# Optimization experiments

Measured on AMD Instinct MI355X. Metric: run time of the kernel, lower is better.

Reference implementation:

```python
import jax, jax.numpy as jnp
import numpy as np

N_NODES = 10000
N_EDGES = 640000
MODEL_DIM = 128
HIDDEN = [128, 128]


def setup_inputs() -> dict:
    key = jax.random.key(0)
    ks = jax.random.split(key, 10)
    node_feature = jax.random.normal(ks[0], (N_NODES, MODEL_DIM), dtype=jnp.float32)
    src = jax.random.randint(ks[1], (N_EDGES,), 0, N_NODES, dtype=jnp.int32)
    dst = jax.random.randint(ks[2], (N_EDGES,), 0, N_NODES, dtype=jnp.int32)
    in_dim = 2 * MODEL_DIM  # concat(aggregated_message, node_feature)
    # MLP: in_dim -> 128 -> 128 -> MODEL_DIM, ReLU between hidden layers
    W1 = jax.random.normal(ks[3], (in_dim, HIDDEN[0]), dtype=jnp.float32) / np.sqrt(in_dim)
    b1 = jnp.zeros((HIDDEN[0],), dtype=jnp.float32)
    W2 = jax.random.normal(ks[4], (HIDDEN[0], HIDDEN[1]), dtype=jnp.float32) / np.sqrt(HIDDEN[0])
    b2 = jnp.zeros((HIDDEN[1],), dtype=jnp.float32)
    W3 = jax.random.normal(ks[5], (HIDDEN[1], MODEL_DIM), dtype=jnp.float32) / np.sqrt(HIDDEN[1])
    b3 = jnp.zeros((MODEL_DIM,), dtype=jnp.float32)
    return {"node_feature": node_feature, "src": src, "dst": dst,
            "W1": W1, "b1": b1, "W2": W2, "b2": b2, "W3": W3, "b3": b3}


def reference(node_feature, src, dst, W1, b1, W2, b2, W3, b3):
    # message: gather src node features along edges  [E, D]
    # reduce: sum messages into dst nodes            [N, D]
    agg = jax.ops.segment_sum(node_feature[src], dst, num_segments=N_NODES)
    # apply_node_function_yes_neighbor: concat(aggregated_message, node_feature) -> MLP
    x = jnp.concatenate([agg, node_feature], axis=-1)  # [N, 2D]
    h = jax.nn.relu(x @ W1 + b1)
    h = jax.nn.relu(h @ W2 + b2)
    out = h @ W3 + b3  # [N, D]
    return out
```

## Files before the change

### kernel.cpp

```cpp
#include <hip/hip_runtime.h>
#include <hip/hip_bf16.h>

#define MODEL_D 128
#define CHUNK_SHIFT 13
#define CHUNK_SZ (1 << CHUNK_SHIFT)
#define CAPN 160
#define LDS_HIST 10240

typedef unsigned short ushort_t;
typedef unsigned int uint_t;
typedef __attribute__((ext_vector_type(8))) short short8v;
typedef __attribute__((ext_vector_type(4))) float f32x4;

static __device__ __forceinline__ ushort_t f2b(float v) {
    __hip_bfloat16 h = __float2bfloat16(v);
    return *reinterpret_cast<ushort_t*>(&h);
}

static __device__ __forceinline__ void acc8(float* acc, uint4 wv) {
    union { uint_t u32; float f; } lo, hi;
    lo.u32 = wv.x << 16;          acc[0] += lo.f;
    hi.u32 = wv.x & 0xffff0000u;  acc[1] += hi.f;
    lo.u32 = wv.y << 16;          acc[2] += lo.f;
    hi.u32 = wv.y & 0xffff0000u;  acc[3] += hi.f;
    lo.u32 = wv.z << 16;          acc[4] += lo.f;
    hi.u32 = wv.z & 0xffff0000u;  acc[5] += hi.f;
    lo.u32 = wv.w << 16;          acc[6] += lo.f;
    hi.u32 = wv.w & 0xffff0000u;  acc[7] += hi.f;
}

__global__ __launch_bounds__(1024) void histrank_convert_kernel(
    const int* __restrict__ dst, int* __restrict__ rank,
    int* __restrict__ hist2,
    const float* __restrict__ feat,
    const float* __restrict__ W1, const float* __restrict__ W2,
    const float* __restrict__ W3,
    ushort_t* __restrict__ featB, ushort_t* __restrict__ W1t,
    ushort_t* __restrict__ W2t, ushort_t* __restrict__ W3t,
    int E, int N, int nFeat, int C)
{
    __shared__ int h[LDS_HIST];
    const int t = threadIdx.x;
    const int c = blockIdx.x;

    if (c < C) {
        for (int i = t; i < N; i += 1024) h[i] = 0;
        __syncthreads();
        int e0 = c << CHUNK_SHIFT;
        int e1 = min(e0 + CHUNK_SZ, E);
        for (int e = e0 + t; e < e1; e += 1024)
            rank[e] = atomicAdd(&h[dst[e]], 1);
        __syncthreads();
        for (int i = t; i < N; i += 1024) hist2[(size_t)c * N + i] = h[i];
    }

    int gid = blockIdx.x * 1024 + t;
    int stride = gridDim.x * 1024;
    const int n1 = 256 * 128, n2 = 128 * 128, n3 = 128 * 128;
    int total = nFeat + n1 + n2 + n3;
    for (int i = gid; i < total; i += stride) {
        if (i < nFeat) {
            featB[i] = f2b(feat[i]);
        } else if (i < nFeat + n1) {
            int idx = i - nFeat; int j = idx >> 8, k = idx & 255;
            W1t[idx] = f2b(W1[k * 128 + j]);
        } else if (i < nFeat + n1 + n2) {
            int idx = i - nFeat - n1; int j = idx >> 7, k = idx & 127;
            W2t[idx] = f2b(W2[k * 128 + j]);
        } else {
            int idx = i - nFeat - n1 - n2; int j = idx >> 7, k = idx & 127;
            W3t[idx] = f2b(W3[k * 128 + j]);
        }
    }
}

__global__ __launch_bounds__(1024) void chunkscan_kernel(
    const int* __restrict__ hist2, int* __restrict__ chunkOff,
    int* __restrict__ deg, int N, int C)
{
    int node = blockIdx.x * 1024 + threadIdx.x;
    if (node >= N) return;
    int acc = 0;
    #pragma unroll 4
    for (int c = 0; c < C; ++c) {
        int v = hist2[(size_t)c * N + node];
        chunkOff[(size_t)c * N + node] = acc;
        acc += v;
    }
    deg[node] = acc;
}

__global__ __launch_bounds__(1024) void fill_kernel(
    const int* __restrict__ src, const int* __restrict__ dst,
    const int* __restrict__ rank, const int* __restrict__ chunkOff,
    int* __restrict__ srcSorted, int E, int N)
{
    int gid = blockIdx.x * 1024 + threadIdx.x;
    int stride = gridDim.x * 1024;
    for (int e = gid; e < E; e += stride) {
        int d = dst[e];
        int c = e >> CHUNK_SHIFT;
        int off = chunkOff[(size_t)c * N + d] + rank[e];
        if (off < CAPN) srcSorted[d * CAPN + off] = src[e];
    }
}

__global__ __launch_bounds__(512) void agg_mlp_kernel(
    const ushort_t* __restrict__ featB,
    const int* __restrict__ deg, const int* __restrict__ srcSorted,
    const ushort_t* __restrict__ W1t, const ushort_t* __restrict__ W2t,
    const ushort_t* __restrict__ W3t,
    const float* __restrict__ b1, const float* __restrict__ b2,
    const float* __restrict__ b3,
    float* __restrict__ out, int N)
{
    __shared__ ushort_t xsh[16][136];
    __shared__ ushort_t h1[16][136];
    __shared__ ushort_t h2[16][136];

    const int t = threadIdx.x;
    const int lane = t & 63;
    const int w = t >> 6;
    const int nb0 = blockIdx.x * 16;

    const int g4 = lane >> 4;
    const int c16 = lane & 15;
    const size_t cOff = c16 * 8;

    for (int q = 0; q < 2; ++q) {
        const int nl = w * 2 + q;
        const int node = nb0 + nl;
        float acc[8];
        #pragma unroll
        for (int j = 0; j < 8; ++j) acc[j] = 0.f;

        int degN = 0;
        if (node < N) {
            degN = deg[node];
            degN = (degN < CAPN) ? degN : CAPN;
        }
        const int sbase = node * CAPN;

        for (int chunk = 0; chunk < degN; chunk += 64) {
            int e = chunk + lane;
            int myidx = (e < degN) ? srcSorted[sbase + e] : 0;
            int nact = degN - chunk;
            nact = (nact < 64) ? nact : 64;
            int nfull = nact >> 2;

            int u = 0;
            for (; u + 4 <= nfull; u += 4) {
                int s0 = __shfl(myidx, (u + 0) * 4 + g4);
                int s1 = __shfl(myidx, (u + 1) * 4 + g4);
                int s2 = __shfl(myidx, (u + 2) * 4 + g4);
                int s3 = __shfl(myidx, (u + 3) * 4 + g4);
                uint4 wv0 = *(const uint4*)(featB + (size_t)s0 * MODEL_D + cOff);
                uint4 wv1 = *(const uint4*)(featB + (size_t)s1 * MODEL_D + cOff);
                uint4 wv2 = *(const uint4*)(featB + (size_t)s2 * MODEL_D + cOff);
                uint4 wv3 = *(const uint4*)(featB + (size_t)s3 * MODEL_D + cOff);
                acc8(acc, wv0);
                acc8(acc, wv1);
                acc8(acc, wv2);
                acc8(acc, wv3);
            }
            for (; u < nfull; ++u) {
                int s = __shfl(myidx, u * 4 + g4);
                uint4 wv = *(const uint4*)(featB + (size_t)s * MODEL_D + cOff);
                acc8(acc, wv);
            }
            int rem = nact & 3;
            if (rem) {
                bool valid = g4 < rem;
                int sel = valid ? (nfull * 4 + g4) : 0;
                int s = __shfl(myidx, sel);
                uint4 wv = *(const uint4*)(featB + (size_t)s * MODEL_D + cOff);
                if (valid) acc8(acc, wv);
            }
        }

        #pragma unroll
        for (int j = 0; j < 8; ++j) {
            acc[j] += __shfl_xor(acc[j], 16);
            acc[j] += __shfl_xor(acc[j], 32);
        }

        if (lane < 16) {
            uint4 o;
            o.x = (uint_t)f2b(acc[0]) | ((uint_t)f2b(acc[1]) << 16);
            o.y = (uint_t)f2b(acc[2]) | ((uint_t)f2b(acc[3]) << 16);
            o.z = (uint_t)f2b(acc[4]) | ((uint_t)f2b(acc[5]) << 16);
            o.w = (uint_t)f2b(acc[6]) | ((uint_t)f2b(acc[7]) << 16);
            *(uint4*)((char*)&xsh[nl][0] + c16 * 16) = o;
        }
    }
    __syncthreads();

    const int r16 = lane & 15;
    const int g = lane >> 4;
    const int ct = w;
    const int nodeA = nb0 + r16;
    const int nodeAc = (nodeA < N) ? nodeA : (N - 1);

    short8v a1f[8];
    {
        #pragma unroll
        for (int ks = 0; ks < 4; ++ks)
            a1f[ks] = *(const short8v*)&xsh[r16][ks * 32 + g * 8];
        #pragma unroll
        for (int ks = 0; ks < 4; ++ks)
            a1f[4 + ks] = *(const short8v*)(featB + (size_t)nodeAc * MODEL_D + ks * 32 + g * 8);

        f32x4 c = {0.f, 0.f, 0.f, 0.f};
        #pragma unroll
        for (int ks = 0; ks < 8; ++ks) {
            short8v b = *(const short8v*)(W1t + (ct * 16 + r16) * 256 + ks * 32 + g * 8);
            c = __builtin_amdgcn_mfma_f32_16x16x32_bf16(a1f[ks], b, c, 0, 0, 0);
        }
        const float bias = b1[ct * 16 + r16];
        #pragma unroll
        for (int i = 0; i < 4; ++i) {
            float v = fmaxf(c[i] + bias, 0.f);
            h1[g * 4 + i][ct * 16 + r16] = f2b(v);
        }
    }
    __syncthreads();

    {
        short8v a2f[4];
        #pragma unroll
        for (int ks = 0; ks < 4; ++ks)
            a2f[ks] = *(const short8v*)&h1[r16][ks * 32 + g * 8];
        f32x4 c = {0.f, 0.f, 0.f, 0.f};
        #pragma unroll
        for (int ks = 0; ks < 4; ++ks) {
            short8v b = *(const short8v*)(W2t + (ct * 16 + r16) * 128 + ks * 32 + g * 8);
            c = __builtin_amdgcn_mfma_f32_16x16x32_bf16(a2f[ks], b, c, 0, 0, 0);
        }
        const float bias = b2[ct * 16 + r16];
        #pragma unroll
        for (int i = 0; i < 4; ++i) {
            float v = fmaxf(c[i] + bias, 0.f);
            h2[g * 4 + i][ct * 16 + r16] = f2b(v);
        }
    }
    __syncthreads();

    {
        short8v a3f[4];
        #pragma unroll
        for (int ks = 0; ks < 4; ++ks)
            a3f[ks] = *(const short8v*)&h2[r16][ks * 32 + g * 8];
        f32x4 c = {0.f, 0.f, 0.f, 0.f};
        #pragma unroll
        for (int ks = 0; ks < 4; ++ks) {
            short8v b = *(const short8v*)(W3t + (ct * 16 + r16) * 128 + ks * 32 + g * 8);
            c = __builtin_amdgcn_mfma_f32_16x16x32_bf16(a3f[ks], b, c, 0, 0, 0);
        }
        const float bias = b3[ct * 16 + r16];
        #pragma unroll
        for (int i = 0; i < 4; ++i) {
            int node = nb0 + g * 4 + i;
            if (node < N)
                out[(size_t)node * MODEL_D + ct * 16 + r16] = c[i] + bias;
        }
    }
}

extern "C" void kernel_launch(void* const* d_in, const int* in_sizes, int n_in,
                              void* d_out, int out_size, void* d_ws, size_t ws_size,
                              hipStream_t stream) {
    const float* feat = (const float*)d_in[0];
    const int*   src  = (const int*)d_in[1];
    const int*   dst  = (const int*)d_in[2];
    const float* W1   = (const float*)d_in[3];
    const float* b1   = (const float*)d_in[4];
    const float* W2   = (const float*)d_in[5];
    const float* b2   = (const float*)d_in[6];
    const float* W3   = (const float*)d_in[7];
    const float* b3   = (const float*)d_in[8];
    float* out = (float*)d_out;

    const int N = in_sizes[0] / MODEL_D;
    const int E = in_sizes[1];
    const int NFEAT = N * MODEL_D;
    const int C = (E + CHUNK_SZ - 1) >> CHUNK_SHIFT;

    ushort_t* featB = (ushort_t*)d_ws;
    ushort_t* W1t   = featB + NFEAT;
    ushort_t* W2t   = W1t + 256 * 128;
    ushort_t* W3t   = W2t + 128 * 128;
    int* rank       = (int*)(W3t + 128 * 128);
    int* hist2      = rank + E;
    int* chunkOff   = hist2 + (size_t)C * N;
    int* deg        = chunkOff + (size_t)C * N;
    int* srcSorted  = deg + N;

    histrank_convert_kernel<<<625, 1024, 0, stream>>>(
        dst, rank, hist2, feat, W1, W2, W3,
        featB, W1t, W2t, W3t, E, N, NFEAT, C);

    chunkscan_kernel<<<(N + 1023) / 1024, 1024, 0, stream>>>(
        hist2, chunkOff, deg, N, C);

    fill_kernel<<<625, 1024, 0, stream>>>(
        src, dst, rank, chunkOff, srcSorted, E, N);

    agg_mlp_kernel<<<(N + 15) / 16, 512, 0, stream>>>(
        featB, deg, srcSorted, W1t, W2t, W3t, b1, b2, b3, out, N);
}
```

Measured before the change: 62.26 us.

## Split fused aggregation+MLP into separate gather kernel and 64-node MLP kernel

Splits the fused aggregate-and-MLP kernel into two kernels. The first gathers and sums neighbor features with one wave per node and writes the bf16 aggregate to workspace. The second runs the three-layer MLP on 64-node tiles, keeping weight fragments in registers and reusing them across four 16-row sub-tiles, which cuts repeated weight loads and removes the block-wide sync after the irregular gather. In exchange it adds an extra kernel launch and a round trip of the aggregate through global memory.

```diff
diff --git a/kernel.cpp b/kernel.cpp
--- a/kernel.cpp
+++ b/kernel.cpp
@@ -105,163 +105,202 @@
     }
 }
 
-__global__ __launch_bounds__(512) void agg_mlp_kernel(
+__global__ __launch_bounds__(256) void agg_kernel(
     const ushort_t* __restrict__ featB,
     const int* __restrict__ deg, const int* __restrict__ srcSorted,
+    ushort_t* __restrict__ aggB, int N)
+{
+    int gid = blockIdx.x * 256 + threadIdx.x;
+    int node = gid >> 6;
+    if (node >= N) return;
+    int lane = gid & 63;
+    const int g4 = lane >> 4;
+    const int c16 = lane & 15;
+    const size_t cOff = c16 * 8;
+
+    float acc[8];
+    #pragma unroll
+    for (int j = 0; j < 8; ++j) acc[j] = 0.f;
+
+    int degN = deg[node];
+    degN = (degN < CAPN) ? degN : CAPN;
+    const int sbase = node * CAPN;
+
+    for (int chunk = 0; chunk < degN; chunk += 64) {
+        int e = chunk + lane;
+        int myidx = (e < degN) ? srcSorted[sbase + e] : 0;
+        int nact = degN - chunk;
+        nact = (nact < 64) ? nact : 64;
+        int nfull = nact >> 2;
+
+        int u = 0;
+        for (; u + 4 <= nfull; u += 4) {
+            int s0 = __shfl(myidx, (u + 0) * 4 + g4);
+            int s1 = __shfl(myidx, (u + 1) * 4 + g4);
+            int s2 = __shfl(myidx, (u + 2) * 4 + g4);
+            int s3 = __shfl(myidx, (u + 3) * 4 + g4);
+            uint4 wv0 = *(const uint4*)(featB + (size_t)s0 * MODEL_D + cOff);
+            uint4 wv1 = *(const uint4*)(featB + (size_t)s1 * MODEL_D + cOff);
+            uint4 wv2 = *(const uint4*)(featB + (size_t)s2 * MODEL_D + cOff);
+            uint4 wv3 = *(const uint4*)(featB + (size_t)s3 * MODEL_D + cOff);
+            acc8(acc, wv0);
+            acc8(acc, wv1);
+            acc8(acc, wv2);
+            acc8(acc, wv3);
+        }
+        for (; u < nfull; ++u) {
+            int s = __shfl(myidx, u * 4 + g4);
+            uint4 wv = *(const uint4*)(featB + (size_t)s * MODEL_D + cOff);
+            acc8(acc, wv);
+        }
+        int rem = nact & 3;
+        if (rem) {
+            bool valid = g4 < rem;
+            int sel = valid ? (nfull * 4 + g4) : 0;
+            int s = __shfl(myidx, sel);
+            uint4 wv = *(const uint4*)(featB + (size_t)s * MODEL_D + cOff);
+            if (valid) acc8(acc, wv);
+        }
+    }
+
+    #pragma unroll
+    for (int j = 0; j < 8; ++j) {
+        acc[j] += __shfl_xor(acc[j], 16);
+        acc[j] += __shfl_xor(acc[j], 32);
+    }
+
+    if (lane < 16) {
+        uint4 o;
+        o.x = (uint_t)f2b(acc[0]) | ((uint_t)f2b(acc[1]) << 16);
+        o.y = (uint_t)f2b(acc[2]) | ((uint_t)f2b(acc[3]) << 16);
+        o.z = (uint_t)f2b(acc[4]) | ((uint_t)f2b(acc[5]) << 16);
+        o.w = (uint_t)f2b(acc[6]) | ((uint_t)f2b(acc[7]) << 16);
+        *(uint4*)(aggB + (size_t)node * MODEL_D + c16 * 8) = o;
+    }
+}
+
+__global__ __launch_bounds__(256) void mlp_kernel(
+    const ushort_t* __restrict__ aggB, const ushort_t* __restrict__ featB,
     const ushort_t* __restrict__ W1t, const ushort_t* __restrict__ W2t,
     const ushort_t* __restrict__ W3t,
     const float* __restrict__ b1, const float* __restrict__ b2,
     const float* __restrict__ b3,
     float* __restrict__ out, int N)
 {
-    __shared__ ushort_t xsh[16][136];
-    __shared__ ushort_t h1[16][136];
-    __shared__ ushort_t h2[16][136];
+    __shared__ ushort_t h1[64][136];
+    __shared__ ushort_t h2[64][136];
 
     const int t = threadIdx.x;
     const int lane = t & 63;
     const int w = t >> 6;
-    const int nb0 = blockIdx.x * 16;
-
-    const int g4 = lane >> 4;
-    const int c16 = lane & 15;
-    const size_t cOff = c16 * 8;
-
-    for (int q = 0; q < 2; ++q) {
-        const int nl = w * 2 + q;
-        const int node = nb0 + nl;
-        float acc[8];
-        #pragma unroll
-        for (int j = 0; j < 8; ++j) acc[j] = 0.f;
-
-        int degN = 0;
-        if (node < N) {
-            degN = deg[node];
-            degN = (degN < CAPN) ? degN : CAPN;
-        }
-        const int sbase = node * CAPN;
-
-        for (int chunk = 0; chunk < degN; chunk += 64) {
-            int e = chunk + lane;
-            int myidx = (e < degN) ? srcSorted[sbase + e] : 0;
-            int nact = degN - chunk;
-            nact = (nact < 64) ? nact : 64;
-            int nfull = nact >> 2;
-
-            int u = 0;
-            for (; u + 4 <= nfull; u += 4) {
-                int s0 = __shfl(myidx, (u + 0) * 4 + g4);
-                int s1 = __shfl(myidx, (u + 1) * 4 + g4);
-                int s2 = __shfl(myidx, (u + 2) * 4 + g4);
-                int s3 = __shfl(myidx, (u + 3) * 4 + g4);
-                uint4 wv0 = *(const uint4*)(featB + (size_t)s0 * MODEL_D + cOff);
-                uint4 wv1 = *(const uint4*)(featB + (size_t)s1 * MODEL_D + cOff);
-                uint4 wv2 = *(const uint4*)(featB + (size_t)s2 * MODEL_D + cOff);
-                uint4 wv3 = *(const uint4*)(featB + (size_t)s3 * MODEL_D + cOff);
-                acc8(acc, wv0);
-                acc8(acc, wv1);
-                acc8(acc, wv2);
-                acc8(acc, wv3);
-            }
-            for (; u < nfull; ++u) {
-                int s = __shfl(myidx, u * 4 + g4);
-                uint4 wv = *(const uint4*)(featB + (size_t)s * MODEL_D + cOff);
-                acc8(acc, wv);
-            }
-            int rem = nact & 3;
-            if (rem) {
-                bool valid = g4 < rem;
-                int sel = valid ? (nfull * 4 + g4) : 0;
-                int s = __shfl(myidx, sel);
-                uint4 wv = *(const uint4*)(featB + (size_t)s * MODEL_D + cOff);
-                if (valid) acc8(acc, wv);
-            }
-        }
-
-        #pragma unroll
-        for (int j = 0; j < 8; ++j) {
-            acc[j] += __shfl_xor(acc[j], 16);
-            acc[j] += __shfl_xor(acc[j], 32);
-        }
-
-        if (lane < 16) {
-            uint4 o;
-            o.x = (uint_t)f2b(acc[0]) | ((uint_t)f2b(acc[1]) << 16);
-            o.y = (uint_t)f2b(acc[2]) | ((uint_t)f2b(acc[3]) << 16);
-            o.z = (uint_t)f2b(acc[4]) | ((uint_t)f2b(acc[5]) << 16);
-            o.w = (uint_t)f2b(acc[6]) | ((uint_t)f2b(acc[7]) << 16);
-            *(uint4*)((char*)&xsh[nl][0] + c16 * 16) = o;
-        }
-    }
-    __syncthreads();
-
     const int r16 = lane & 15;
     const int g = lane >> 4;
-    const int ct = w;
-    const int nodeA = nb0 + r16;
-    const int nodeAc = (nodeA < N) ? nodeA : (N - 1);
-
-    short8v a1f[8];
+    const int nb0 = blockIdx.x * 64;
+
     {
-        #pragma unroll
-        for (int ks = 0; ks < 4; ++ks)
-            a1f[ks] = *(const short8v*)&xsh[r16][ks * 32 + g * 8];
-        #pragma unroll
-        for (int ks = 0; ks < 4; ++ks)
-            a1f[4 + ks] = *(const short8v*)(featB + (size_t)nodeAc * MODEL_D + ks * 32 + g * 8);
-
-        f32x4 c = {0.f, 0.f, 0.f, 0.f};
-        #pragma unroll
-        for (int ks = 0; ks < 8; ++ks) {
-            short8v b = *(const short8v*)(W1t + (ct * 16 + r16) * 256 + ks * 32 + g * 8);
-            c = __builtin_amdgcn_mfma_f32_16x16x32_bf16(a1f[ks], b, c, 0, 0, 0);
-        }
-        const float bias = b1[ct * 16 + r16];
-        #pragma unroll
-        for (int i = 0; i < 4; ++i) {
-            float v = fmaxf(c[i] + bias, 0.f);
-            h1[g * 4 + i][ct * 16 + r16] = f2b(v);
+        short8v B1[2][8];
+        float bias1[2];
+        #pragma unroll
+        for (int cc = 0; cc < 2; ++cc) {
+            const int ct = w * 2 + cc;
+            #pragma unroll
+            for (int ks = 0; ks < 8; ++ks)
+                B1[cc][ks] = *(const short8v*)(W1t + (ct * 16 + r16) * 256 + ks * 32 + g * 8);
+            bias1[cc] = b1[ct * 16 + r16];
+        }
+        #pragma unroll
+        for (int b = 0; b < 4; ++b) {
+            int nodeA = nb0 + b * 16 + r16;
+            int nodeAc = (nodeA < N) ? nodeA : (N - 1);
+            short8v a1f[8];
+            #pragma unroll
+            for (int ks = 0; ks < 4; ++ks)
+                a1f[ks] = *(const short8v*)(aggB + (size_t)nodeAc * MODEL_D + ks * 32 + g * 8);
+            #pragma unroll
+            for (int ks = 0; ks < 4; ++ks)
+                a1f[4 + ks] = *(const short8v*)(featB + (size_t)nodeAc * MODEL_D + ks * 32 + g * 8);
+            #pragma unroll
+            for (int cc = 0; cc < 2; ++cc) {
+                const int ct = w * 2 + cc;
+                f32x4 c = {0.f, 0.f, 0.f, 0.f};
+                #pragma unroll
+                for (int ks = 0; ks < 8; ++ks)
+                    c = __builtin_amdgcn_mfma_f32_16x16x32_bf16(a1f[ks], B1[cc][ks], c, 0, 0, 0);
+                #pragma unroll
+                for (int i = 0; i < 4; ++i) {
+                    float v = fmaxf(c[i] + bias1[cc], 0.f);
+                    h1[b * 16 + g * 4 + i][ct * 16 + r16] = f2b(v);
+                }
+            }
         }
     }
     __syncthreads();
 
     {
-        short8v a2f[4];
-        #pragma unroll
-        for (int ks = 0; ks < 4; ++ks)
-            a2f[ks] = *(const short8v*)&h1[r16][ks * 32 + g * 8];
-        f32x4 c = {0.f, 0.f, 0.f, 0.f};
-        #pragma unroll
-        for (int ks = 0; ks < 4; ++ks) {
-            short8v b = *(const short8v*)(W2t + (ct * 16 + r16) * 128 + ks * 32 + g * 8);
-            c = __builtin_amdgcn_mfma_f32_16x16x32_bf16(a2f[ks], b, c, 0, 0, 0);
-        }
-        const float bias = b2[ct * 16 + r16];
-        #pragma unroll
-        for (int i = 0; i < 4; ++i) {
-            float v = fmaxf(c[i] + bias, 0.f);
-            h2[g * 4 + i][ct * 16 + r16] = f2b(v);
+        short8v B2[2][4];
+        float bias2[2];
+        #pragma unroll
+        for (int cc = 0; cc < 2; ++cc) {
+            const int ct = w * 2 + cc;
+            #pragma unroll
+            for (int ks = 0; ks < 4; ++ks)
+                B2[cc][ks] = *(const short8v*)(W2t + (ct * 16 + r16) * 128 + ks * 32 + g * 8);
+            bias2[cc] = b2[ct * 16 + r16];
+        }
+        #pragma unroll
+        for (int b = 0; b < 4; ++b) {
+            short8v a2f[4];
+            #pragma unroll
+            for (int ks = 0; ks < 4; ++ks)
+                a2f[ks] = *(const short8v*)&h1[b * 16 + r16][ks * 32 + g * 8];
+            #pragma unroll
+            for (int cc = 0; cc < 2; ++cc) {
+                const int ct = w * 2 + cc;
+                f32x4 c = {0.f, 0.f, 0.f, 0.f};
+                #pragma unroll
+                for (int ks = 0; ks < 4; ++ks)
+                    c = __builtin_amdgcn_mfma_f32_16x16x32_bf16(a2f[ks], B2[cc][ks], c, 0, 0, 0);
+                #pragma unroll
+                for (int i = 0; i < 4; ++i) {
+                    float v = fmaxf(c[i] + bias2[cc], 0.f);
+                    h2[b * 16 + g * 4 + i][ct * 16 + r16] = f2b(v);
+                }
+            }
         }
     }
     __syncthreads();
 
     {
-        short8v a3f[4];
-        #pragma unroll
-        for (int ks = 0; ks < 4; ++ks)
-            a3f[ks] = *(const short8v*)&h2[r16][ks * 32 + g * 8];
-        f32x4 c = {0.f, 0.f, 0.f, 0.f};
-        #pragma unroll
-        for (int ks = 0; ks < 4; ++ks) {
-            short8v b = *(const short8v*)(W3t + (ct * 16 + r16) * 128 + ks * 32 + g * 8);
-            c = __builtin_amdgcn_mfma_f32_16x16x32_bf16(a3f[ks], b, c, 0, 0, 0);
-        }
-        const float bias = b3[ct * 16 + r16];
-        #pragma unroll
-        for (int i = 0; i < 4; ++i) {
-            int node = nb0 + g * 4 + i;
-            if (node < N)
-                out[(size_t)node * MODEL_D + ct * 16 + r16] = c[i] + bias;
+        short8v B3[2][4];
+        float bias3[2];
+        #pragma unroll
+        for (int cc = 0; cc < 2; ++cc) {
+            const int ct = w * 2 + cc;
+            #pragma unroll
+            for (int ks = 0; ks < 4; ++ks)
+                B3[cc][ks] = *(const short8v*)(W3t + (ct * 16 + r16) * 128 + ks * 32 + g * 8);
+            bias3[cc] = b3[ct * 16 + r16];
+        }
+        #pragma unroll
+        for (int b = 0; b < 4; ++b) {
+            short8v a3f[4];
+            #pragma unroll
+            for (int ks = 0; ks < 4; ++ks)
+                a3f[ks] = *(const short8v*)&h2[b * 16 + r16][ks * 32 + g * 8];
+            #pragma unroll
+            for (int cc = 0; cc < 2; ++cc) {
+                const int ct = w * 2 + cc;
+                f32x4 c = {0.f, 0.f, 0.f, 0.f};
+                #pragma unroll
+                for (int ks = 0; ks < 4; ++ks)
+                    c = __builtin_amdgcn_mfma_f32_16x16x32_bf16(a3f[ks], B3[cc][ks], c, 0, 0, 0);
+                #pragma unroll
+                for (int i = 0; i < 4; ++i) {
+                    int node = nb0 + b * 16 + g * 4 + i;
+                    if (node < N)
+                        out[(size_t)node * MODEL_D + ct * 16 + r16] = c[i] + bias3[cc];
+                }
+            }
         }
     }
 }
@@ -286,7 +325,8 @@
     const int C = (E + CHUNK_SZ - 1) >> CHUNK_SHIFT;
 
     ushort_t* featB = (ushort_t*)d_ws;
-    ushort_t* W1t   = featB + NFEAT;
+    ushort_t* aggB  = featB + NFEAT;
+    ushort_t* W1t   = aggB + NFEAT;
     ushort_t* W2t   = W1t + 256 * 128;
     ushort_t* W3t   = W2t + 128 * 128;
     int* rank       = (int*)(W3t + 128 * 128);
@@ -305,6 +345,9 @@
     fill_kernel<<<625, 1024, 0, stream>>>(
         src, dst, rank, chunkOff, srcSorted, E, N);
 
-    agg_mlp_kernel<<<(N + 15) / 16, 512, 0, stream>>>(
-        featB, deg, srcSorted, W1t, W2t, W3t, b1, b2, b3, out, N);
-}
+    agg_kernel<<<(N * 64 + 255) / 256, 256, 0, stream>>>(
+        featB, deg, srcSorted, aggB, N);
+
+    mlp_kernel<<<(N + 63) / 64, 256, 0, stream>>>(
+        aggB, featB, W1t, W2t, W3t, b1, b2, b3, out, N);
+}
```

Measured after the change: 59.94 us, median of 2. 1.04x faster.

## Split aggregation from MLP into separate kernels and unroll fill by four

Applied to the files above, without the earlier changes.

The fused aggregate+MLP kernel becomes two kernels. A standalone agg_kernel runs one wavefront per node in small blocks and writes bf16 aggregates to a new workspace buffer, and mlp_kernel reads them back from global memory. This targets poor latency hiding and load imbalance in the fused kernel, where each 512-thread block gathered 16 nodes before its MFMA stage. It costs an extra launch and a round trip of the aggregate through memory. Separately, fill_kernel now processes four strided edges per thread to raise memory-level parallelism.

```diff
diff --git a/kernel.cpp b/kernel.cpp
--- a/kernel.cpp
+++ b/kernel.cpp
@@ -96,8 +96,27 @@
     int* __restrict__ srcSorted, int E, int N)
 {
     int gid = blockIdx.x * 1024 + threadIdx.x;
+    int q = E >> 2;
     int stride = gridDim.x * 1024;
-    for (int e = gid; e < E; e += stride) {
+    for (int i = gid; i < q; i += stride) {
+        int e0 = i, e1 = i + q, e2 = i + 2 * q, e3 = i + 3 * q;
+        int d0 = dst[e0], d1 = dst[e1], d2 = dst[e2], d3 = dst[e3];
+        int r0 = rank[e0], r1 = rank[e1], r2 = rank[e2], r3 = rank[e3];
+        int c0 = e0 >> CHUNK_SHIFT, c1 = e1 >> CHUNK_SHIFT;
+        int c2 = e2 >> CHUNK_SHIFT, c3 = e3 >> CHUNK_SHIFT;
+        int o0 = chunkOff[(size_t)c0 * N + d0] + r0;
+        int o1 = chunkOff[(size_t)c1 * N + d1] + r1;
+        int o2 = chunkOff[(size_t)c2 * N + d2] + r2;
+        int o3 = chunkOff[(size_t)c3 * N + d3] + r3;
+        int s0 = src[e0], s1 = src[e1], s2 = src[e2], s3 = src[e3];
+        if (o0 < CAPN) srcSorted[d0 * CAPN + o0] = s0;
+        if (o1 < CAPN) srcSorted[d1 * CAPN + o1] = s1;
+        if (o2 < CAPN) srcSorted[d2 * CAPN + o2] = s2;
+        if (o3 < CAPN) srcSorted[d3 * CAPN + o3] = s3;
+    }
+    int rem = E - 4 * q;
+    if (gid < rem) {
+        int e = 4 * q + gid;
         int d = dst[e];
         int c = e >> CHUNK_SHIFT;
         int off = chunkOff[(size_t)c * N + d] + rank[e];
@@ -105,111 +124,109 @@
     }
 }
 
-__global__ __launch_bounds__(512) void agg_mlp_kernel(
+__global__ __launch_bounds__(256) void agg_kernel(
     const ushort_t* __restrict__ featB,
     const int* __restrict__ deg, const int* __restrict__ srcSorted,
+    ushort_t* __restrict__ aggB, int N)
+{
+    int gid = blockIdx.x * 256 + threadIdx.x;
+    int node = gid >> 6;
+    if (node >= N) return;
+    int lane = gid & 63;
+    const int g4 = lane >> 4;
+    const int c16 = lane & 15;
+    const size_t cOff = c16 * 8;
+
+    float acc[8];
+    #pragma unroll
+    for (int j = 0; j < 8; ++j) acc[j] = 0.f;
+
+    int degN = deg[node];
+    degN = (degN < CAPN) ? degN : CAPN;
+    const int sbase = node * CAPN;
+
+    for (int chunk = 0; chunk < degN; chunk += 64) {
+        int e = chunk + lane;
+        int myidx = (e < degN) ? srcSorted[sbase + e] : 0;
+        int nact = degN - chunk;
+        nact = (nact < 64) ? nact : 64;
+        int nfull = nact >> 2;
+
+        int u = 0;
+        for (; u + 4 <= nfull; u += 4) {
+            int s0 = __shfl(myidx, (u + 0) * 4 + g4);
+            int s1 = __shfl(myidx, (u + 1) * 4 + g4);
+            int s2 = __shfl(myidx, (u + 2) * 4 + g4);
+            int s3 = __shfl(myidx, (u + 3) * 4 + g4);
+            uint4 wv0 = *(const uint4*)(featB + (size_t)s0 * MODEL_D + cOff);
+            uint4 wv1 = *(const uint4*)(featB + (size_t)s1 * MODEL_D + cOff);
+            uint4 wv2 = *(const uint4*)(featB + (size_t)s2 * MODEL_D + cOff);
+            uint4 wv3 = *(const uint4*)(featB + (size_t)s3 * MODEL_D + cOff);
+            acc8(acc, wv0);
+            acc8(acc, wv1);
+            acc8(acc, wv2);
+            acc8(acc, wv3);
+        }
+        for (; u < nfull; ++u) {
+            int s = __shfl(myidx, u * 4 + g4);
+            uint4 wv = *(const uint4*)(featB + (size_t)s * MODEL_D + cOff);
+            acc8(acc, wv);
+        }
+        int rem = nact & 3;
+        if (rem) {
+            bool valid = g4 < rem;
+            int sel = valid ? (nfull * 4 + g4) : 0;
+            int s = __shfl(myidx, sel);
+            uint4 wv = *(const uint4*)(featB + (size_t)s * MODEL_D + cOff);
+            if (valid) acc8(acc, wv);
+        }
+    }
+
+    #pragma unroll
+    for (int j = 0; j < 8; ++j) {
+        acc[j] += __shfl_xor(acc[j], 16);
+        acc[j] += __shfl_xor(acc[j], 32);
+    }
+
+    if (lane < 16) {
+        uint4 o;
+        o.x = (uint_t)f2b(acc[0]) | ((uint_t)f2b(acc[1]) << 16);
+        o.y = (uint_t)f2b(acc[2]) | ((uint_t)f2b(acc[3]) << 16);
+        o.z = (uint_t)f2b(acc[4]) | ((uint_t)f2b(acc[5]) << 16);
+        o.w = (uint_t)f2b(acc[6]) | ((uint_t)f2b(acc[7]) << 16);
+        *(uint4*)(aggB + (size_t)node * MODEL_D + c16 * 8) = o;
+    }
+}
+
+__global__ __launch_bounds__(512) void mlp_kernel(
+    const ushort_t* __restrict__ aggB, const ushort_t* __restrict__ featB,
     const ushort_t* __restrict__ W1t, const ushort_t* __restrict__ W2t,
     const ushort_t* __restrict__ W3t,
     const float* __restrict__ b1, const float* __restrict__ b2,
     const float* __restrict__ b3,
     float* __restrict__ out, int N)
 {
-    __shared__ ushort_t xsh[16][136];
     __shared__ ushort_t h1[16][136];
     __shared__ ushort_t h2[16][136];
 
     const int t = threadIdx.x;
     const int lane = t & 63;
     const int w = t >> 6;
-    const int nb0 = blockIdx.x * 16;
-
-    const int g4 = lane >> 4;
-    const int c16 = lane & 15;
-    const size_t cOff = c16 * 8;
-
-    for (int q = 0; q < 2; ++q) {
-        const int nl = w * 2 + q;
-        const int node = nb0 + nl;
-        float acc[8];
-        #pragma unroll
-        for (int j = 0; j < 8; ++j) acc[j] = 0.f;
-
-        int degN = 0;
-        if (node < N) {
-            degN = deg[node];
-            degN = (degN < CAPN) ? degN : CAPN;
-        }
-        const int sbase = node * CAPN;
-
-        for (int chunk = 0; chunk < degN; chunk += 64) {
-            int e = chunk + lane;
-            int myidx = (e < degN) ? srcSorted[sbase + e] : 0;
-            int nact = degN - chunk;
-            nact = (nact < 64) ? nact : 64;
-            int nfull = nact >> 2;
-
-            int u = 0;
-            for (; u + 4 <= nfull; u += 4) {
-                int s0 = __shfl(myidx, (u + 0) * 4 + g4);
-                int s1 = __shfl(myidx, (u + 1) * 4 + g4);
-                int s2 = __shfl(myidx, (u + 2) * 4 + g4);
-                int s3 = __shfl(myidx, (u + 3) * 4 + g4);
-                uint4 wv0 = *(const uint4*)(featB + (size_t)s0 * MODEL_D + cOff);
-                uint4 wv1 = *(const uint4*)(featB + (size_t)s1 * MODEL_D + cOff);
-                uint4 wv2 = *(const uint4*)(featB + (size_t)s2 * MODEL_D + cOff);
-                uint4 wv3 = *(const uint4*)(featB + (size_t)s3 * MODEL_D + cOff);
-                acc8(acc, wv0);
-                acc8(acc, wv1);
-                acc8(acc, wv2);
-                acc8(acc, wv3);
-            }
-            for (; u < nfull; ++u) {
-                int s = __shfl(myidx, u * 4 + g4);
-                uint4 wv = *(const uint4*)(featB + (size_t)s * MODEL_D + cOff);
-                acc8(acc, wv);
-            }
-            int rem = nact & 3;
-            if (rem) {
-                bool valid = g4 < rem;
-                int sel = valid ? (nfull * 4 + g4) : 0;
-                int s = __shfl(myidx, sel);
-                uint4 wv = *(const uint4*)(featB + (size_t)s * MODEL_D + cOff);
-                if (valid) acc8(acc, wv);
-            }
-        }
-
-        #pragma unroll
-        for (int j = 0; j < 8; ++j) {
-            acc[j] += __shfl_xor(acc[j], 16);
-            acc[j] += __shfl_xor(acc[j], 32);
-        }
-
-        if (lane < 16) {
-            uint4 o;
-            o.x = (uint_t)f2b(acc[0]) | ((uint_t)f2b(acc[1]) << 16);
-            o.y = (uint_t)f2b(acc[2]) | ((uint_t)f2b(acc[3]) << 16);
-            o.z = (uint_t)f2b(acc[4]) | ((uint_t)f2b(acc[5]) << 16);
-            o.w = (uint_t)f2b(acc[6]) | ((uint_t)f2b(acc[7]) << 16);
-            *(uint4*)((char*)&xsh[nl][0] + c16 * 16) = o;
-        }
-    }
-    __syncthreads();
-
     const int r16 = lane & 15;
     const int g = lane >> 4;
     const int ct = w;
+    const int nb0 = blockIdx.x * 16;
     const int nodeA = nb0 + r16;
     const int nodeAc = (nodeA < N) ? nodeA : (N - 1);
 
-    short8v a1f[8];
     {
+        short8v a1f[8];
         #pragma unroll
         for (int ks = 0; ks < 4; ++ks)
-            a1f[ks] = *(const short8v*)&xsh[r16][ks * 32 + g * 8];
+            a1f[ks] = *(const short8v*)(aggB + (size_t)nodeAc * MODEL_D + ks * 32 + g * 8);
         #pragma unroll
         for (int ks = 0; ks < 4; ++ks)
             a1f[4 + ks] = *(const short8v*)(featB + (size_t)nodeAc * MODEL_D + ks * 32 + g * 8);
-
         f32x4 c = {0.f, 0.f, 0.f, 0.f};
         #pragma unroll
         for (int ks = 0; ks < 8; ++ks) {
@@ -286,7 +303,8 @@
     const int C = (E + CHUNK_SZ - 1) >> CHUNK_SHIFT;
 
     ushort_t* featB = (ushort_t*)d_ws;
-    ushort_t* W1t   = featB + NFEAT;
+    ushort_t* aggB  = featB + NFEAT;
+    ushort_t* W1t   = aggB + NFEAT;
     ushort_t* W2t   = W1t + 256 * 128;
     ushort_t* W3t   = W2t + 128 * 128;
     int* rank       = (int*)(W3t + 128 * 128);
@@ -302,9 +320,12 @@
     chunkscan_kernel<<<(N + 1023) / 1024, 1024, 0, stream>>>(
         hist2, chunkOff, deg, N, C);
 
-    fill_kernel<<<625, 1024, 0, stream>>>(
+    fill_kernel<<<((E >> 2) + 1023) / 1024, 1024, 0, stream>>>(
         src, dst, rank, chunkOff, srcSorted, E, N);
 
-    agg_mlp_kernel<<<(N + 15) / 16, 512, 0, stream>>>(
-        featB, deg, srcSorted, W1t, W2t, W3t, b1, b2, b3, out, N);
-}
+    agg_kernel<<<(N * 64 + 255) / 256, 256, 0, stream>>>(
+        featB, deg, srcSorted, aggB, N);
+
+    mlp_kernel<<<(N + 15) / 16, 512, 0, stream>>>(
+        aggB, featB, W1t, W2t, W3t, b1, b2, b3, out, N);
+}
```

After: 68.32 us. +9.7%, slower.
